# Performance work log

Measured on AMD Instinct MI355X. Metric: run time of the kernel, lower is better.

## Reference

```python
import jax, jax.numpy as jnp
import numpy as np

EMBED_DIM = 256
NUM_HEADS = 4
HEAD_DIM = EMBED_DIM // NUM_HEADS
B, N0, N1 = 4, 2048, 2048


def setup_inputs() -> dict:
    key = jax.random.key(0)
    ks = jax.random.split(key, 16)
    d = EMBED_DIM
    s = 0.02
    return {
        "x0": jax.random.normal(ks[0], (B, N0, d), jnp.float32),
        "x1": jax.random.normal(ks[1], (B, N1, d), jnp.float32),
        "Wqk": jax.random.normal(ks[2], (d, d), jnp.float32) * s,
        "bqk": jnp.zeros((d,), jnp.float32),
        "Wv": jax.random.normal(ks[3], (d, d), jnp.float32) * s,
        "bv": jnp.zeros((d,), jnp.float32),
        "Wout": jax.random.normal(ks[4], (d, d), jnp.float32) * s,
        "bout": jnp.zeros((d,), jnp.float32),
        "W0": jax.random.normal(ks[5], (2 * d, 2 * d), jnp.float32) * s,
        "b0": jnp.zeros((2 * d,), jnp.float32),
        "ln_scale": jnp.ones((2 * d,), jnp.float32),
        "ln_bias": jnp.zeros((2 * d,), jnp.float32),
        "W3": jax.random.normal(ks[6], (2 * d, d), jnp.float32) * s,
        "b3": jnp.zeros((d,), jnp.float32),
    }


def _heads(t, b, n):
    # [b, n, d] -> [b, h, n, hd]
    return t.reshape(b, n, NUM_HEADS, HEAD_DIM).transpose(0, 2, 1, 3)


def _layernorm(y, scale, bias, eps=1e-5):
    mu = jnp.mean(y, axis=-1, keepdims=True)
    var = jnp.mean(jnp.square(y - mu), axis=-1, keepdims=True)
    return (y - mu) * jax.lax.rsqrt(var + eps) * scale + bias


def reference(x0, x1, Wqk, bqk, Wv, bv, Wout, bout, W0, b0, ln_scale, ln_bias, W3, b3):
    b, n0, d = x0.shape
    _, n1, _ = x1.shape
    scale = 1.0 / jnp.sqrt(jnp.float32(HEAD_DIM))

    qk0 = _heads(x0 @ Wqk + bqk, b, n0)
    qk1 = _heads(x1 @ Wqk + bqk, b, n1)
    v0 = _heads(x0 @ Wv + bv, b, n0)
    v1 = _heads(x1 @ Wv + bv, b, n1)

    # shared logits: [b, h, n0, n1]
    logits01 = jnp.einsum('bhid,bhjd->bhij', qk0, qk1) * scale
    attn01 = jax.nn.softmax(logits01, axis=-1)
    m0 = jnp.einsum('bhij,bhjd->bhid', attn01, v1)
    attn10 = jax.nn.softmax(logits01.transpose(0, 1, 3, 2), axis=-1)
    m1 = jnp.einsum('bhji,bhjd->bhid', attn10.transpose(0, 1, 3, 2), v0)

    m0 = m0.transpose(0, 2, 1, 3).reshape(b, n0, d) @ Wout + bout
    m1 = m1.transpose(0, 2, 1, 3).reshape(b, n1, d) @ Wout + bout

    def ffn(x, m):
        y = jnp.concatenate([x, m], axis=-1) @ W0 + b0
        y = _layernorm(y, ln_scale, ln_bias)
        y = jax.nn.gelu(y, approximate=False)
        return x + y @ W3 + b3

    return ffn(x0, m0), ffn(x1, m1)
```

## Files before the change

### kernel.cpp

```cpp
#include <hip/hip_runtime.h>
#include <math.h>

#define BATCH 4
#define SEQ 2048
#define DMODEL 256
#define NH 4
#define HD 64
#define MROWS 8192
#define QKSCALE 0.4246608905f

typedef short bf16x8 __attribute__((ext_vector_type(8)));
typedef float f32x4 __attribute__((ext_vector_type(4)));
typedef unsigned short us;

__device__ __forceinline__ us f2bf(float x) {
  union { float f; unsigned int u; } v;
  v.f = x;
  unsigned int r = (v.u + 0x7FFF + ((v.u >> 16) & 1)) >> 16;
  return (us)r;
}
__device__ __forceinline__ us f2bf_trunc(float x) {
  union { float f; unsigned int u; } v;
  v.f = x;
  return (us)(v.u >> 16);
}
__device__ __forceinline__ float bf2f(us u) {
  union { unsigned int u; float f; } v;
  v.u = ((unsigned int)u) << 16;
  return v.f;
}
__device__ __forceinline__ void dma16(const void* g, void* l) {
  auto gp = (const __attribute__((address_space(1))) unsigned int*)(unsigned long long)(uintptr_t)g;
  auto lp = (__attribute__((address_space(3))) unsigned int*)(unsigned int)(uintptr_t)l;
  __builtin_amdgcn_global_load_lds(gp, lp, 16, 0, 0);
}

__global__ __launch_bounds__(256) void cast_x(
    const float* __restrict__ x0, const float* __restrict__ x1,
    us* __restrict__ x0b, us* __restrict__ x1b) {
  const int n4 = (MROWS * DMODEL) / 4;
  int i = blockIdx.x * 256 + threadIdx.x;
  const float* src = (i < n4) ? x0 : x1;
  us* dst = (i < n4) ? x0b : x1b;
  int j = (i < n4) ? i : i - n4;
  float4 v = *(const float4*)&src[j * 4];
  ushort4 o = {f2bf(v.x), f2bf(v.y), f2bf(v.z), f2bf(v.w)};
  *(ushort4*)&dst[j * 4] = o;
}

__global__ __launch_bounds__(256) void cast_w(
    const float* __restrict__ Wqk, const float* __restrict__ Wv,
    const float* __restrict__ W0, const float* __restrict__ W3,
    const float* __restrict__ bqk, const float* __restrict__ bv,
    us* __restrict__ Wqvt, us* __restrict__ W1t, us* __restrict__ W3t,
    float* __restrict__ bias_qv) {
  int gid = blockIdx.x * 256 + threadIdx.x;
  if (gid < 65536) {
    int k = gid >> 8, j = gid & 255;
    Wqvt[j * 256 + k] = f2bf(Wqk[gid]);
  } else if (gid < 131072) {
    int i = gid - 65536;
    int k = i >> 8, j = i & 255;
    Wqvt[(256 + j) * 256 + k] = f2bf(Wv[i]);
  } else if (gid < 262144) {
    int i = gid - 131072;
    int k = i >> 9, j = i & 511;
    W1t[j * 512 + k] = f2bf(W0[i]);
  } else if (gid < 393216) {
    int i = gid - 262144;
    int k = i >> 8, j = i & 255;
    W3t[j * 512 + k] = f2bf(W3[i]);
  } else if (gid < 393728) {
    int j = gid - 393216;
    bias_qv[j] = (j < 256) ? bqk[j] : bv[j - 256];
  }
}

__global__ __launch_bounds__(256) void wcomb_k(
    const float* __restrict__ Wout, const float* __restrict__ W0,
    const float* __restrict__ b0, const float* __restrict__ bout,
    us* __restrict__ W1t, float* __restrict__ bias1) {
  int t = threadIdx.x, i = blockIdx.x;
  if (i < 256) {
    float a0 = 0.f, a1 = 0.f;
    for (int k = 0; k < 256; ++k) {
      float wk = Wout[i * 256 + k];
      const float* row = &W0[(256 + k) * 512];
      a0 += wk * row[t];
      a1 += wk * row[t + 256];
    }
    W1t[t * 512 + 256 + i] = f2bf(a0);
    W1t[(t + 256) * 512 + 256 + i] = f2bf(a1);
  } else {
    float a0 = b0[t], a1 = b0[t + 256];
    for (int k = 0; k < 256; ++k) {
      float bk = bout[k];
      const float* row = &W0[(256 + k) * 512];
      a0 += bk * row[t];
      a1 += bk * row[t + 256];
    }
    bias1[t] = a0;
    bias1[t + 256] = a1;
  }
}

template <int MODE>
__global__ __launch_bounds__(256) void gemm3(
    const us* __restrict__ A0, const us* __restrict__ A1,
    const us* __restrict__ Am0, const us* __restrict__ Am1,
    const us* __restrict__ Wt, const float* __restrict__ bias,
    const float* __restrict__ r0_, const float* __restrict__ r1_,
    void* __restrict__ C0_, void* __restrict__ C1_,
    void* __restrict__ V0_, void* __restrict__ V1_, int K) {
  __shared__ us lds[8192];
  const int t = threadIdx.x, w = t >> 6, lane = t & 63;
  const int qd = lane >> 4, l15 = lane & 15;
  const int row0 = blockIdx.x * 64;
  const int coltile = blockIdx.y, col0 = coltile * 64;
  const int z = blockIdx.z;
  const us* Ax = z ? A1 : A0;
  const us* Am = z ? Am1 : Am0;

  f32x4 acc[4];
#pragma unroll
  for (int tn = 0; tn < 4; ++tn) acc[tn] = (f32x4){0.f, 0.f, 0.f, 0.f};

  for (int k0 = 0; k0 < K; k0 += 64) {
    __syncthreads();
#pragma unroll
    for (int pp = 0; pp < 4; ++pp) {
      int g = pp * 4 + w;
      const us* src;
      if (g < 8) {
        int tm = g >> 1, s = g & 1;
        const us* Ap = Ax;
        int kk = k0 + s * 32 + qd * 8;
        int lda = K;
        if (MODE == 1) {
          Ap = (k0 < 256) ? Ax : Am;
          kk = kk & 255;
          lda = 256;
        }
        src = &Ap[(size_t)(row0 + tm * 16 + l15) * lda + kk];
      } else {
        int tn = (g - 8) >> 1, s = g & 1;
        src = &Wt[(size_t)(col0 + tn * 16 + l15) * K + k0 + s * 32 + qd * 8];
      }
      dma16(src, &lds[g * 512]);
    }
    __syncthreads();

    bf16x8 aA0 = *(const bf16x8*)&lds[((w * 2 + 0) * 64 + lane) * 8];
    bf16x8 aA1 = *(const bf16x8*)&lds[((w * 2 + 1) * 64 + lane) * 8];
#pragma unroll
    for (int tn = 0; tn < 4; ++tn) {
      bf16x8 b0v = *(const bf16x8*)&lds[((8 + tn * 2 + 0) * 64 + lane) * 8];
      bf16x8 b1v = *(const bf16x8*)&lds[((8 + tn * 2 + 1) * 64 + lane) * 8];
      acc[tn] = __builtin_amdgcn_mfma_f32_16x16x32_bf16(aA0, b0v, acc[tn], 0, 0, 0);
      acc[tn] = __builtin_amdgcn_mfma_f32_16x16x32_bf16(aA1, b1v, acc[tn], 0, 0, 0);
    }
  }

  if (MODE == 0) {
    if (coltile < 4) {
      us* C = (us*)(z ? C1_ : C0_);
#pragma unroll
      for (int tn = 0; tn < 4; ++tn) {
        int col = col0 + tn * 16 + l15;
        float bb = bias[col];
#pragma unroll
        for (int r = 0; r < 4; ++r) {
          size_t grow = row0 + w * 16 + qd * 4 + r;
          C[grow * 256 + col] = f2bf((acc[tn][r] + bb) * QKSCALE);
        }
      }
    } else {
      __syncthreads();
      int h_ = coltile - 4;
#pragma unroll
      for (int tn = 0; tn < 4; ++tn) {
        int col = col0 + tn * 16 + l15;
        float bb = bias[col];
#pragma unroll
        for (int r = 0; r < 4; ++r) {
          int rloc = w * 16 + qd * 4 + r;
          lds[(tn * 16 + l15) * 66 + rloc] = f2bf(acc[tn][r] + bb);
        }
      }
      __syncthreads();
      us* Vt = (us*)(z ? V1_ : V0_);
      int b_ = row0 >> 11, seq0 = row0 & 2047;
      for (int c = t; c < 512; c += 256) {
        int dloc = c >> 3, scc = c & 7;
        uint4 d = *(const uint4*)&lds[dloc * 66 + scc * 8];
        *(uint4*)&Vt[((size_t)(b_ * NH + h_) * HD + dloc) * SEQ + seq0 + scc * 8] = d;
      }
    }
  } else if (MODE == 1) {
    us* C = (us*)(z ? C1_ : C0_);
#pragma unroll
    for (int tn = 0; tn < 4; ++tn) {
      int col = col0 + tn * 16 + l15;
      float bb = bias[col];
#pragma unroll
      for (int r = 0; r < 4; ++r) {
        size_t grow = row0 + w * 16 + qd * 4 + r;
        C[grow * 512 + col] = f2bf(acc[tn][r] + bb);
      }
    }
  } else {
    float* C = (float*)(z ? C1_ : C0_);
    const float* R = z ? r1_ : r0_;
#pragma unroll
    for (int tn = 0; tn < 4; ++tn) {
      int col = col0 + tn * 16 + l15;
      float bb = bias[col];
#pragma unroll
      for (int r = 0; r < 4; ++r) {
        size_t grow = row0 + w * 16 + qd * 4 + r;
        C[grow * 256 + col] = R[grow * 256 + col] + acc[tn][r] + bb;
      }
    }
  }
}

__global__ __launch_bounds__(256) void flash_v5(
    const us* __restrict__ qk0, const us* __restrict__ qk1,
    const us* __restrict__ vt0, const us* __restrict__ vt1,
    float* __restrict__ Opart, float* __restrict__ lpart) {
  __shared__ us lds[8192];
  const int t = threadIdx.x, w = t >> 6, lane = t & 63;
  const int qd = lane >> 4, l15 = lane & 15;
  const int qt = blockIdx.x & 15, half = blockIdx.x >> 4;
  const int h = blockIdx.y, z = blockIdx.z, dir = z & 1, b = z >> 1;
  const us* Qb = dir ? qk1 : qk0;
  const us* Kb = dir ? qk0 : qk1;
  const us* Vt = dir ? vt0 : vt1;
  float* Op = Opart + (size_t)(dir * 2 + half) * (MROWS * DMODEL);
  float* lp = lpart + ((size_t)(dir * 2 + half) * NH + h) * MROWS;
  const size_t qrow0 = (size_t)b * SEQ + (size_t)qt * 128;
  const int hoff = h * HD;
  const us* vtb = Vt + (size_t)(b * NH + h) * HD * SEQ;

  bf16x8 qf[2][2];
#pragma unroll
  for (int qh = 0; qh < 2; ++qh)
#pragma unroll
    for (int s = 0; s < 2; ++s)
      qf[qh][s] = *(const bf16x8*)&Qb[(qrow0 + w * 32 + qh * 16 + l15) * DMODEL + hoff + s * 32 + qd * 8];

  f32x4 Oacc[2][4];
#pragma unroll
  for (int qh = 0; qh < 2; ++qh)
#pragma unroll
    for (int td = 0; td < 4; ++td) Oacc[qh][td] = (f32x4){0.f, 0.f, 0.f, 0.f};
  float l_lane[2] = {0.f, 0.f};

  for (int kt = half * 16; kt < half * 16 + 16; ++kt) {
    const size_t kbase = (size_t)b * SEQ + (size_t)kt * 64;
    __syncthreads();
#pragma unroll
    for (int pp = 0; pp < 4; ++pp) {
      int g = pp * 4 + w;
      const us* src;
      if (g < 8) {
        int tk = g >> 1, s = g & 1;
        int kvl = (tk >> 1) * 32 + (l15 >> 2) * 8 + (tk & 1) * 4 + (l15 & 3);
        src = &Kb[(kbase + kvl) * DMODEL + hoff + s * 32 + qd * 8];
      } else {
        int td = (g - 8) >> 1, s = g & 1;
        src = &vtb[(size_t)(td * 16 + l15) * SEQ + kt * 64 + s * 32 + qd * 8];
      }
      dma16(src, &lds[g * 512]);
    }
    __syncthreads();

    bf16x8 kf[4][2], vf[4][2];
#pragma unroll
    for (int tk = 0; tk < 4; ++tk)
#pragma unroll
      for (int s = 0; s < 2; ++s) {
        kf[tk][s] = *(const bf16x8*)&lds[((tk * 2 + s) * 64 + lane) * 8];
        vf[tk][s] = *(const bf16x8*)&lds[((8 + tk * 2 + s) * 64 + lane) * 8];
      }

#pragma unroll
    for (int qh = 0; qh < 2; ++qh) {
      f32x4 S[4];
#pragma unroll
      for (int tk = 0; tk < 4; ++tk) {
        f32x4 a = {0.f, 0.f, 0.f, 0.f};
        a = __builtin_amdgcn_mfma_f32_16x16x32_bf16(kf[tk][0], qf[qh][0], a, 0, 0, 0);
        a = __builtin_amdgcn_mfma_f32_16x16x32_bf16(kf[tk][1], qf[qh][1], a, 0, 0, 0);
        S[tk] = a;
      }
      float p[4][4];
      float rs = 0.f;
#pragma unroll
      for (int tk = 0; tk < 4; ++tk)
#pragma unroll
        for (int r = 0; r < 4; ++r) {
          float pv = exp2f(S[tk][r]);
          p[tk][r] = pv;
          rs += pv;
        }
      l_lane[qh] += rs;
      bf16x8 pA[2];
#pragma unroll
      for (int s = 0; s < 2; ++s) {
        bf16x8 v;
#pragma unroll
        for (int j = 0; j < 4; ++j) {
          v[j] = (short)f2bf_trunc(p[2 * s][j]);
          v[j + 4] = (short)f2bf_trunc(p[2 * s + 1][j]);
        }
        pA[s] = v;
      }
#pragma unroll
      for (int td = 0; td < 4; ++td) {
        Oacc[qh][td] = __builtin_amdgcn_mfma_f32_16x16x32_bf16(pA[0], vf[td][0], Oacc[qh][td], 0, 0, 0);
        Oacc[qh][td] = __builtin_amdgcn_mfma_f32_16x16x32_bf16(pA[1], vf[td][1], Oacc[qh][td], 0, 0, 0);
      }
    }
  }

#pragma unroll
  for (int qh = 0; qh < 2; ++qh) {
    float l = l_lane[qh];
    l += __shfl_xor(l, 16);
    l += __shfl_xor(l, 32);
    if (qd == 0) lp[qrow0 + w * 32 + qh * 16 + l15] = l;
#pragma unroll
    for (int r = 0; r < 4; ++r) {
      size_t row = qrow0 + w * 32 + qh * 16 + qd * 4 + r;
#pragma unroll
      for (int td = 0; td < 4; ++td)
        Op[row * DMODEL + hoff + td * 16 + l15] = Oacc[qh][td][r];
    }
  }
}

__global__ __launch_bounds__(256) void combine_k(
    const float* __restrict__ Opart, const float* __restrict__ lpart,
    us* __restrict__ m0b, us* __restrict__ m1b) {
  int gid = blockIdx.x * 256 + threadIdx.x;
  int dir = gid >= (MROWS * DMODEL / 4);
  int idx = gid - dir * (MROWS * DMODEL / 4);
  int row = idx >> 6;
  int c4 = (idx & 63) << 2;
  int h = c4 >> 6;
  const float* Oa = Opart + (size_t)(dir * 2 + 0) * (MROWS * DMODEL);
  const float* Ob = Opart + (size_t)(dir * 2 + 1) * (MROWS * DMODEL);
  float la = lpart[((size_t)(dir * 2 + 0) * NH + h) * MROWS + row];
  float lb = lpart[((size_t)(dir * 2 + 1) * NH + h) * MROWS + row];
  float inv = 1.0f / (la + lb);
  float4 a = *(const float4*)&Oa[(size_t)row * DMODEL + c4];
  float4 bv = *(const float4*)&Ob[(size_t)row * DMODEL + c4];
  us* m = dir ? m1b : m0b;
  ushort4 o = {f2bf((a.x + bv.x) * inv), f2bf((a.y + bv.y) * inv),
               f2bf((a.z + bv.z) * inv), f2bf((a.w + bv.w) * inv)};
  *(ushort4*)&m[(size_t)row * DMODEL + c4] = o;
}

__global__ __launch_bounds__(256) void ln_gelu3(
    us* __restrict__ Y0, us* __restrict__ Y1,
    const float* __restrict__ sc, const float* __restrict__ bi) {
  int w = threadIdx.x >> 6, lane = threadIdx.x & 63;
  int ridx = blockIdx.x * 4 + w;
  us* Y = (ridx >= MROWS) ? Y1 : Y0;
  int row = ridx & (MROWS - 1);
  us* p = Y + (size_t)row * 512 + lane * 8;
  uint4 u = *(const uint4*)p;
  unsigned int uu[4] = {u.x, u.y, u.z, u.w};
  float v[8];
#pragma unroll
  for (int i = 0; i < 4; ++i) {
    v[2 * i] = bf2f((us)(uu[i] & 0xFFFF));
    v[2 * i + 1] = bf2f((us)(uu[i] >> 16));
  }
  float s1 = 0.f, s2 = 0.f;
#pragma unroll
  for (int i = 0; i < 8; ++i) { s1 += v[i]; s2 += v[i] * v[i]; }
#pragma unroll
  for (int m = 1; m < 64; m <<= 1) {
    s1 += __shfl_xor(s1, m);
    s2 += __shfl_xor(s2, m);
  }
  float mu = s1 * (1.0f / 512.0f);
  float var = s2 * (1.0f / 512.0f) - mu * mu;
  float rstd = rsqrtf(var + 1e-5f);
  int c0 = lane * 8;
  float4 scA = *(const float4*)&sc[c0], scB = *(const float4*)&sc[c0 + 4];
  float4 biA = *(const float4*)&bi[c0], biB = *(const float4*)&bi[c0 + 4];
  float scv[8] = {scA.x, scA.y, scA.z, scA.w, scB.x, scB.y, scB.z, scB.w};
  float biv[8] = {biA.x, biA.y, biA.z, biA.w, biB.x, biB.y, biB.z, biB.w};
  unsigned int ou[4];
#pragma unroll
  for (int i = 0; i < 4; ++i) {
    float y0 = (v[2 * i] - mu) * rstd * scv[2 * i] + biv[2 * i];
    float y1 = (v[2 * i + 1] - mu) * rstd * scv[2 * i + 1] + biv[2 * i + 1];
    y0 = 0.5f * y0 * (1.0f + erff(y0 * 0.70710678118654752f));
    y1 = 0.5f * y1 * (1.0f + erff(y1 * 0.70710678118654752f));
    ou[i] = (unsigned int)f2bf(y0) | ((unsigned int)f2bf(y1) << 16);
  }
  uint4 o = {ou[0], ou[1], ou[2], ou[3]};
  *(uint4*)p = o;
}

extern "C" void kernel_launch(void* const* d_in, const int* in_sizes, int n_in,
                              void* d_out, int out_size, void* d_ws,
                              size_t ws_size, hipStream_t stream) {
  const float* x0   = (const float*)d_in[0];
  const float* x1   = (const float*)d_in[1];
  const float* Wqk  = (const float*)d_in[2];
  const float* bqk  = (const float*)d_in[3];
  const float* Wv   = (const float*)d_in[4];
  const float* bv   = (const float*)d_in[5];
  const float* Wout = (const float*)d_in[6];
  const float* bout = (const float*)d_in[7];
  const float* W0   = (const float*)d_in[8];
  const float* b0   = (const float*)d_in[9];
  const float* lns  = (const float*)d_in[10];
  const float* lnb  = (const float*)d_in[11];
  const float* W3   = (const float*)d_in[12];
  const float* b3   = (const float*)d_in[13];

  char* ws = (char*)d_ws;
  const size_t MB = 1024 * 1024;
  us* x0b  = (us*)(ws + 0 * MB);
  us* x1b  = (us*)(ws + 4 * MB);
  us* Wqvt = (us*)(ws + 8 * MB);
  us* W1t  = (us*)(ws + 8 * MB + 262144);
  us* W3t  = (us*)(ws + 8 * MB + 786432);
  float* bias_qv = (float*)(ws + 9 * MB);
  float* bias1   = (float*)(ws + 9 * MB + 4096);
  us* qk0b = (us*)(ws + 10 * MB);
  us* qk1b = (us*)(ws + 14 * MB);
  us* vt0  = (us*)(ws + 18 * MB);
  us* vt1  = (us*)(ws + 22 * MB);
  us* m0b  = (us*)(ws + 26 * MB);
  us* m1b  = (us*)(ws + 30 * MB);
  us* y0b  = (us*)(ws + 10 * MB);
  us* y1b  = (us*)(ws + 18 * MB);
  float* Opart = (float*)(ws + 34 * MB);
  float* lpart = (float*)(ws + 66 * MB);
  float* out0 = (float*)d_out;
  float* out1 = out0 + (size_t)MROWS * DMODEL;

  dim3 blk(256);

  cast_x<<<dim3(4096), blk, 0, stream>>>(x0, x1, x0b, x1b);
  cast_w<<<dim3(1538), blk, 0, stream>>>(Wqk, Wv, W0, W3, bqk, bv,
                                         Wqvt, W1t, W3t, bias_qv);
  wcomb_k<<<dim3(257), blk, 0, stream>>>(Wout, W0, b0, bout, W1t, bias1);

  gemm3<0><<<dim3(128, 8, 2), blk, 0, stream>>>(
      x0b, x1b, nullptr, nullptr, Wqvt, bias_qv, nullptr, nullptr,
      qk0b, qk1b, vt0, vt1, 256);

  flash_v5<<<dim3(32, 4, 8), blk, 0, stream>>>(qk0b, qk1b, vt0, vt1, Opart, lpart);
  combine_k<<<dim3(4096), blk, 0, stream>>>(Opart, lpart, m0b, m1b);

  gemm3<1><<<dim3(128, 8, 2), blk, 0, stream>>>(
      x0b, x1b, m0b, m1b, W1t, bias1, nullptr, nullptr,
      y0b, y1b, nullptr, nullptr, 512);

  ln_gelu3<<<dim3(4096), blk, 0, stream>>>(y0b, y1b, lns, lnb);

  gemm3<2><<<dim3(128, 4, 2), blk, 0, stream>>>(
      y0b, y1b, nullptr, nullptr, W3t, b3, x0, x1,
      out0, out1, nullptr, nullptr, 512);
}
```

Before: 268.5 us.

## Enlarge GEMM tiles to 128x128, double-buffer flash K/V loads, cheaper exp/pack

The GEMM kernels go from 64x64 to 128x128 output tiles, with each wave computing a 4x4 grid of MFMA tiles. This raises data reuse from LDS and halves the grid; the V-transpose epilogue is adjusted to cover two heads per tile. The flash attention kernel double-buffers its K/V tiles in LDS so the next tile's DMA overlaps compute, and it uses the hardware exp2 builtin plus a perm-based bf16 pack for P. The weight-combination kernel also unrolls its reduction loop by 8. The trade-off is more LDS and registers per block, which can reduce occupancy, and fewer blocks for the smaller GEMMs.

New measurement: 229.1 us. 1.17x faster.

```diff
diff --git a/kernel.cpp b/kernel.cpp
--- a/kernel.cpp
+++ b/kernel.cpp
@@ -13,21 +13,30 @@
 typedef float f32x4 __attribute__((ext_vector_type(4)));
 typedef unsigned short us;
 
+#if __has_builtin(__builtin_amdgcn_exp2f)
+#define EXP2(x) __builtin_amdgcn_exp2f(x)
+#else
+#define EXP2(x) exp2f(x)
+#endif
+
 __device__ __forceinline__ us f2bf(float x) {
   union { float f; unsigned int u; } v;
   v.f = x;
   unsigned int r = (v.u + 0x7FFF + ((v.u >> 16) & 1)) >> 16;
   return (us)r;
 }
-__device__ __forceinline__ us f2bf_trunc(float x) {
-  union { float f; unsigned int u; } v;
-  v.f = x;
-  return (us)(v.u >> 16);
-}
 __device__ __forceinline__ float bf2f(us u) {
   union { unsigned int u; float f; } v;
   v.u = ((unsigned int)u) << 16;
   return v.f;
+}
+__device__ __forceinline__ unsigned int fbits(float x) {
+  union { float f; unsigned int u; } v;
+  v.f = x;
+  return v.u;
+}
+__device__ __forceinline__ unsigned int pk2bf(float lo, float hi) {
+  return __builtin_amdgcn_perm(fbits(hi), fbits(lo), 0x07060302u);
 }
 __device__ __forceinline__ void dma16(const void* g, void* l) {
   auto gp = (const __attribute__((address_space(1))) unsigned int*)(unsigned long long)(uintptr_t)g;
@@ -83,11 +92,17 @@
   int t = threadIdx.x, i = blockIdx.x;
   if (i < 256) {
     float a0 = 0.f, a1 = 0.f;
-    for (int k = 0; k < 256; ++k) {
-      float wk = Wout[i * 256 + k];
-      const float* row = &W0[(256 + k) * 512];
-      a0 += wk * row[t];
-      a1 += wk * row[t + 256];
+    for (int k0 = 0; k0 < 256; k0 += 8) {
+      float wk[8], r0[8], r1[8];
+#pragma unroll
+      for (int u = 0; u < 8; ++u) {
+        wk[u] = Wout[i * 256 + k0 + u];
+        const float* row = &W0[(size_t)(256 + k0 + u) * 512];
+        r0[u] = row[t];
+        r1[u] = row[t + 256];
+      }
+#pragma unroll
+      for (int u = 0; u < 8; ++u) { a0 += wk[u] * r0[u]; a1 += wk[u] * r1[u]; }
     }
     W1t[t * 512 + 256 + i] = f2bf(a0);
     W1t[(t + 256) * 512 + 256 + i] = f2bf(a1);
@@ -95,7 +110,7 @@
     float a0 = b0[t], a1 = b0[t + 256];
     for (int k = 0; k < 256; ++k) {
       float bk = bout[k];
-      const float* row = &W0[(256 + k) * 512];
+      const float* row = &W0[(size_t)(256 + k) * 512];
       a0 += bk * row[t];
       a1 += bk * row[t + 256];
     }
@@ -105,33 +120,37 @@
 }
 
 template <int MODE>
-__global__ __launch_bounds__(256) void gemm3(
+__global__ __launch_bounds__(256) void gemm4(
     const us* __restrict__ A0, const us* __restrict__ A1,
     const us* __restrict__ Am0, const us* __restrict__ Am1,
     const us* __restrict__ Wt, const float* __restrict__ bias,
     const float* __restrict__ r0_, const float* __restrict__ r1_,
     void* __restrict__ C0_, void* __restrict__ C1_,
     void* __restrict__ V0_, void* __restrict__ V1_, int K) {
-  __shared__ us lds[8192];
+  __shared__ us lds[17408];
+
   const int t = threadIdx.x, w = t >> 6, lane = t & 63;
   const int qd = lane >> 4, l15 = lane & 15;
-  const int row0 = blockIdx.x * 64;
-  const int coltile = blockIdx.y, col0 = coltile * 64;
+  const int qr = w >> 1, qc = w & 1;
+  const int row0 = blockIdx.x * 128;
+  const int coltile = blockIdx.y, col0 = coltile * 128;
   const int z = blockIdx.z;
   const us* Ax = z ? A1 : A0;
   const us* Am = z ? Am1 : Am0;
 
-  f32x4 acc[4];
-#pragma unroll
-  for (int tn = 0; tn < 4; ++tn) acc[tn] = (f32x4){0.f, 0.f, 0.f, 0.f};
+  f32x4 acc[4][4];
+#pragma unroll
+  for (int i = 0; i < 4; ++i)
+#pragma unroll
+    for (int j = 0; j < 4; ++j) acc[i][j] = (f32x4){0.f, 0.f, 0.f, 0.f};
 
   for (int k0 = 0; k0 < K; k0 += 64) {
     __syncthreads();
 #pragma unroll
-    for (int pp = 0; pp < 4; ++pp) {
+    for (int pp = 0; pp < 8; ++pp) {
       int g = pp * 4 + w;
       const us* src;
-      if (g < 8) {
+      if (g < 16) {
         int tm = g >> 1, s = g & 1;
         const us* Ap = Ax;
         int kk = k0 + s * 32 + qd * 8;
@@ -143,92 +162,83 @@
         }
         src = &Ap[(size_t)(row0 + tm * 16 + l15) * lda + kk];
       } else {
-        int tn = (g - 8) >> 1, s = g & 1;
+        int gb = g - 16, tn = gb >> 1, s = gb & 1;
         src = &Wt[(size_t)(col0 + tn * 16 + l15) * K + k0 + s * 32 + qd * 8];
       }
       dma16(src, &lds[g * 512]);
     }
     __syncthreads();
 
-    bf16x8 aA0 = *(const bf16x8*)&lds[((w * 2 + 0) * 64 + lane) * 8];
-    bf16x8 aA1 = *(const bf16x8*)&lds[((w * 2 + 1) * 64 + lane) * 8];
-#pragma unroll
-    for (int tn = 0; tn < 4; ++tn) {
-      bf16x8 b0v = *(const bf16x8*)&lds[((8 + tn * 2 + 0) * 64 + lane) * 8];
-      bf16x8 b1v = *(const bf16x8*)&lds[((8 + tn * 2 + 1) * 64 + lane) * 8];
-      acc[tn] = __builtin_amdgcn_mfma_f32_16x16x32_bf16(aA0, b0v, acc[tn], 0, 0, 0);
-      acc[tn] = __builtin_amdgcn_mfma_f32_16x16x32_bf16(aA1, b1v, acc[tn], 0, 0, 0);
-    }
-  }
-
-  if (MODE == 0) {
-    if (coltile < 4) {
-      us* C = (us*)(z ? C1_ : C0_);
-#pragma unroll
-      for (int tn = 0; tn < 4; ++tn) {
-        int col = col0 + tn * 16 + l15;
-        float bb = bias[col];
-#pragma unroll
-        for (int r = 0; r < 4; ++r) {
-          size_t grow = row0 + w * 16 + qd * 4 + r;
-          C[grow * 256 + col] = f2bf((acc[tn][r] + bb) * QKSCALE);
+#pragma unroll
+    for (int s = 0; s < 2; ++s) {
+      bf16x8 af[4], bfr[4];
+#pragma unroll
+      for (int i = 0; i < 4; ++i) {
+        af[i] = *(const bf16x8*)&lds[(((qr * 4 + i) * 2 + s) * 64 + lane) * 8];
+        bfr[i] = *(const bf16x8*)&lds[8192 + (((qc * 4 + i) * 2 + s) * 64 + lane) * 8];
+      }
+#pragma unroll
+      for (int i = 0; i < 4; ++i)
+#pragma unroll
+        for (int j = 0; j < 4; ++j)
+          acc[i][j] = __builtin_amdgcn_mfma_f32_16x16x32_bf16(af[i], bfr[j], acc[i][j], 0, 0, 0);
+    }
+  }
+
+  if (MODE == 0 && coltile >= 2) {
+    __syncthreads();
+    int base = qc * 8320;
+#pragma unroll
+    for (int j = 0; j < 4; ++j) {
+      int col = col0 + qc * 64 + j * 16 + l15;
+      float bb = bias[col];
+#pragma unroll
+      for (int i = 0; i < 4; ++i)
+#pragma unroll
+        for (int r = 0; r < 4; ++r)
+          lds[base + (j * 16 + l15) * 130 + (qr * 64 + i * 16 + qd * 4 + r)] =
+              f2bf(acc[i][j][r] + bb);
+    }
+    __syncthreads();
+    us* Vt = (us*)(z ? V1_ : V0_);
+    int b_ = row0 >> 11, seq0 = row0 & 2047;
+    for (int c = t; c < 2048; c += 256) {
+      int hh = c >> 10, cc = c & 1023;
+      int dloc = cc >> 4, scc = cc & 15;
+      int h = (coltile - 2) * 2 + hh;
+      uint4 d = *(const uint4*)&lds[hh * 8320 + dloc * 130 + scc * 8];
+      *(uint4*)&Vt[((size_t)(b_ * NH + h) * HD + dloc) * SEQ + seq0 + scc * 8] = d;
+    }
+    return;
+  }
+
+#pragma unroll
+  for (int j = 0; j < 4; ++j) {
+    int col = col0 + qc * 64 + j * 16 + l15;
+    float bb = bias[col];
+#pragma unroll
+    for (int i = 0; i < 4; ++i)
+#pragma unroll
+      for (int r = 0; r < 4; ++r) {
+        size_t grow = row0 + qr * 64 + i * 16 + qd * 4 + r;
+        float v = acc[i][j][r] + bb;
+        if (MODE == 0) {
+          ((us*)(z ? C1_ : C0_))[grow * 256 + col] = f2bf(v * QKSCALE);
+        } else if (MODE == 1) {
+          ((us*)(z ? C1_ : C0_))[grow * 512 + col] = f2bf(v);
+        } else {
+          const float* R = z ? r1_ : r0_;
+          ((float*)(z ? C1_ : C0_))[grow * 256 + col] = R[grow * 256 + col] + v;
         }
       }
-    } else {
-      __syncthreads();
-      int h_ = coltile - 4;
-#pragma unroll
-      for (int tn = 0; tn < 4; ++tn) {
-        int col = col0 + tn * 16 + l15;
-        float bb = bias[col];
-#pragma unroll
-        for (int r = 0; r < 4; ++r) {
-          int rloc = w * 16 + qd * 4 + r;
-          lds[(tn * 16 + l15) * 66 + rloc] = f2bf(acc[tn][r] + bb);
-        }
-      }
-      __syncthreads();
-      us* Vt = (us*)(z ? V1_ : V0_);
-      int b_ = row0 >> 11, seq0 = row0 & 2047;
-      for (int c = t; c < 512; c += 256) {
-        int dloc = c >> 3, scc = c & 7;
-        uint4 d = *(const uint4*)&lds[dloc * 66 + scc * 8];
-        *(uint4*)&Vt[((size_t)(b_ * NH + h_) * HD + dloc) * SEQ + seq0 + scc * 8] = d;
-      }
-    }
-  } else if (MODE == 1) {
-    us* C = (us*)(z ? C1_ : C0_);
-#pragma unroll
-    for (int tn = 0; tn < 4; ++tn) {
-      int col = col0 + tn * 16 + l15;
-      float bb = bias[col];
-#pragma unroll
-      for (int r = 0; r < 4; ++r) {
-        size_t grow = row0 + w * 16 + qd * 4 + r;
-        C[grow * 512 + col] = f2bf(acc[tn][r] + bb);
-      }
-    }
-  } else {
-    float* C = (float*)(z ? C1_ : C0_);
-    const float* R = z ? r1_ : r0_;
-#pragma unroll
-    for (int tn = 0; tn < 4; ++tn) {
-      int col = col0 + tn * 16 + l15;
-      float bb = bias[col];
-#pragma unroll
-      for (int r = 0; r < 4; ++r) {
-        size_t grow = row0 + w * 16 + qd * 4 + r;
-        C[grow * 256 + col] = R[grow * 256 + col] + acc[tn][r] + bb;
-      }
-    }
-  }
-}
-
-__global__ __launch_bounds__(256) void flash_v5(
+  }
+}
+
+__global__ __launch_bounds__(256) void flash_v6(
     const us* __restrict__ qk0, const us* __restrict__ qk1,
     const us* __restrict__ vt0, const us* __restrict__ vt1,
     float* __restrict__ Opart, float* __restrict__ lpart) {
-  __shared__ us lds[8192];
+  __shared__ us lds[16384];
   const int t = threadIdx.x, w = t >> 6, lane = t & 63;
   const int qd = lane >> 4, l15 = lane & 15;
   const int qt = blockIdx.x & 15, half = blockIdx.x >> 4;
@@ -241,6 +251,24 @@
   const size_t qrow0 = (size_t)b * SEQ + (size_t)qt * 128;
   const int hoff = h * HD;
   const us* vtb = Vt + (size_t)(b * NH + h) * HD * SEQ;
+  const int kt0 = half * 16;
+
+  const us* sp[4];
+  int sstr[4];
+#pragma unroll
+  for (int pp = 0; pp < 4; ++pp) {
+    int g = pp * 4 + w;
+    if (g < 8) {
+      int tk = g >> 1, s = g & 1;
+      int kvl = (tk >> 1) * 32 + (l15 >> 2) * 8 + (tk & 1) * 4 + (l15 & 3);
+      sp[pp] = &Kb[(size_t)(b * SEQ + kt0 * 64 + kvl) * DMODEL + hoff + s * 32 + qd * 8];
+      sstr[pp] = 64 * DMODEL;
+    } else {
+      int td = (g - 8) >> 1, s = g & 1;
+      sp[pp] = &vtb[(size_t)(td * 16 + l15) * SEQ + kt0 * 64 + s * 32 + qd * 8];
+      sstr[pp] = 64;
+    }
+  }
 
   bf16x8 qf[2][2];
 #pragma unroll
@@ -256,32 +284,31 @@
     for (int td = 0; td < 4; ++td) Oacc[qh][td] = (f32x4){0.f, 0.f, 0.f, 0.f};
   float l_lane[2] = {0.f, 0.f};
 
-  for (int kt = half * 16; kt < half * 16 + 16; ++kt) {
-    const size_t kbase = (size_t)b * SEQ + (size_t)kt * 64;
-    __syncthreads();
-#pragma unroll
-    for (int pp = 0; pp < 4; ++pp) {
-      int g = pp * 4 + w;
-      const us* src;
-      if (g < 8) {
-        int tk = g >> 1, s = g & 1;
-        int kvl = (tk >> 1) * 32 + (l15 >> 2) * 8 + (tk & 1) * 4 + (l15 & 3);
-        src = &Kb[(kbase + kvl) * DMODEL + hoff + s * 32 + qd * 8];
-      } else {
-        int td = (g - 8) >> 1, s = g & 1;
-        src = &vtb[(size_t)(td * 16 + l15) * SEQ + kt * 64 + s * 32 + qd * 8];
-      }
-      dma16(src, &lds[g * 512]);
-    }
-    __syncthreads();
+#pragma unroll
+  for (int pp = 0; pp < 4; ++pp) {
+    dma16(sp[pp], &lds[(pp * 4 + w) * 512]);
+    sp[pp] += sstr[pp];
+  }
+  __syncthreads();
+
+  int bsel = 0;
+  for (int it = 0; it < 16; ++it) {
+    if (it < 15) {
+#pragma unroll
+      for (int pp = 0; pp < 4; ++pp) {
+        dma16(sp[pp], &lds[(bsel ^ 1) * 8192 + (pp * 4 + w) * 512]);
+        sp[pp] += sstr[pp];
+      }
+    }
+    const us* L = &lds[bsel * 8192];
 
     bf16x8 kf[4][2], vf[4][2];
 #pragma unroll
     for (int tk = 0; tk < 4; ++tk)
 #pragma unroll
       for (int s = 0; s < 2; ++s) {
-        kf[tk][s] = *(const bf16x8*)&lds[((tk * 2 + s) * 64 + lane) * 8];
-        vf[tk][s] = *(const bf16x8*)&lds[((8 + tk * 2 + s) * 64 + lane) * 8];
+        kf[tk][s] = *(const bf16x8*)&L[((tk * 2 + s) * 64 + lane) * 8];
+        vf[tk][s] = *(const bf16x8*)&L[((8 + tk * 2 + s) * 64 + lane) * 8];
       }
 
 #pragma unroll
@@ -300,28 +327,28 @@
       for (int tk = 0; tk < 4; ++tk)
 #pragma unroll
         for (int r = 0; r < 4; ++r) {
-          float pv = exp2f(S[tk][r]);
+          float pv = EXP2(S[tk][r]);
           p[tk][r] = pv;
           rs += pv;
         }
       l_lane[qh] += rs;
-      bf16x8 pA[2];
-#pragma unroll
-      for (int s = 0; s < 2; ++s) {
-        bf16x8 v;
-#pragma unroll
-        for (int j = 0; j < 4; ++j) {
-          v[j] = (short)f2bf_trunc(p[2 * s][j]);
-          v[j + 4] = (short)f2bf_trunc(p[2 * s + 1][j]);
-        }
-        pA[s] = v;
-      }
+      union { bf16x8 v; unsigned int u[4]; } pk0, pk1;
+      pk0.u[0] = pk2bf(p[0][0], p[0][1]);
+      pk0.u[1] = pk2bf(p[0][2], p[0][3]);
+      pk0.u[2] = pk2bf(p[1][0], p[1][1]);
+      pk0.u[3] = pk2bf(p[1][2], p[1][3]);
+      pk1.u[0] = pk2bf(p[2][0], p[2][1]);
+      pk1.u[1] = pk2bf(p[2][2], p[2][3]);
+      pk1.u[2] = pk2bf(p[3][0], p[3][1]);
+      pk1.u[3] = pk2bf(p[3][2], p[3][3]);
 #pragma unroll
       for (int td = 0; td < 4; ++td) {
-        Oacc[qh][td] = __builtin_amdgcn_mfma_f32_16x16x32_bf16(pA[0], vf[td][0], Oacc[qh][td], 0, 0, 0);
-        Oacc[qh][td] = __builtin_amdgcn_mfma_f32_16x16x32_bf16(pA[1], vf[td][1], Oacc[qh][td], 0, 0, 0);
-      }
-    }
+        Oacc[qh][td] = __builtin_amdgcn_mfma_f32_16x16x32_bf16(pk0.v, vf[td][0], Oacc[qh][td], 0, 0, 0);
+        Oacc[qh][td] = __builtin_amdgcn_mfma_f32_16x16x32_bf16(pk1.v, vf[td][1], Oacc[qh][td], 0, 0, 0);
+      }
+    }
+    __syncthreads();
+    bsel ^= 1;
   }
 
 #pragma unroll
@@ -454,20 +481,20 @@
                                          Wqvt, W1t, W3t, bias_qv);
   wcomb_k<<<dim3(257), blk, 0, stream>>>(Wout, W0, b0, bout, W1t, bias1);
 
-  gemm3<0><<<dim3(128, 8, 2), blk, 0, stream>>>(
+  gemm4<0><<<dim3(64, 4, 2), blk, 0, stream>>>(
       x0b, x1b, nullptr, nullptr, Wqvt, bias_qv, nullptr, nullptr,
       qk0b, qk1b, vt0, vt1, 256);
 
-  flash_v5<<<dim3(32, 4, 8), blk, 0, stream>>>(qk0b, qk1b, vt0, vt1, Opart, lpart);
+  flash_v6<<<dim3(32, 4, 8), blk, 0, stream>>>(qk0b, qk1b, vt0, vt1, Opart, lpart);
   combine_k<<<dim3(4096), blk, 0, stream>>>(Opart, lpart, m0b, m1b);
 
-  gemm3<1><<<dim3(128, 8, 2), blk, 0, stream>>>(
+  gemm4<1><<<dim3(64, 4, 2), blk, 0, stream>>>(
       x0b, x1b, m0b, m1b, W1t, bias1, nullptr, nullptr,
       y0b, y1b, nullptr, nullptr, 512);
 
   ln_gelu3<<<dim3(4096), blk, 0, stream>>>(y0b, y1b, lns, lnb);
 
-  gemm3<2><<<dim3(128, 4, 2), blk, 0, stream>>>(
+  gemm4<2><<<dim3(64, 2, 2), blk, 0, stream>>>(
       y0b, y1b, nullptr, nullptr, W3t, b3, x0, x1,
       out0, out1, nullptr, nullptr, 512);
 }
```
